# Performance work log

Measured on AMD Instinct MI355X. Metric: run time of the kernel, lower is better.

The kernel has to match this reference:

```python
import math
import jax, jax.numpy as jnp
import numpy as np

B, T, D = 4, 4096, 512


def setup_inputs() -> dict:
    key = jax.random.key(0)
    k1, _ = jax.random.split(key)
    x = jax.random.normal(k1, (B, T, D), dtype=jnp.float32)
    log_alpha = jnp.zeros((), dtype=jnp.float32)
    return {"x": x, "log_alpha": log_alpha}


def _gelu_tanh(x):
    c = math.sqrt(2.0 / math.pi)
    return 0.5 * x * (1.0 + jnp.tanh(c * (x + 0.044715 * x * x * x)))


def reference(x, log_alpha):
    Bx, Tx, Dx = x.shape
    alpha = jax.nn.softplus(log_alpha)
    # F.normalize(dim=-1): x / max(||x||, eps)
    norm = jnp.maximum(jnp.linalg.norm(x, axis=-1, keepdims=True), 1e-12)
    x_norm = x / norm
    sim = jnp.einsum("btd,bsd->bts", x_norm, x_norm)  # [B,T,T]
    # causal mask: triu incl. diagonal (col >= row) filled with -2.0
    row = jnp.arange(Tx)[:, None]
    col = jnp.arange(Tx)[None, :]
    mask = col >= row  # [T,T]
    sim = jnp.where(mask[None], jnp.float32(-2.0), sim)
    max_sim = jnp.max(sim, axis=-1)  # [B,T]
    max_sim = jnp.maximum(max_sim, -1.0)
    familiarity = (max_sim + 1.0) * 0.5
    novelty = 1.0 - familiarity
    gate = 1.0 + alpha * novelty[..., None]  # [B,T,1]
    return _gelu_tanh(x * gate)
```

## Files before the change

### kernel.cpp

```cpp
#include <hip/hip_runtime.h>
#include <hip/hip_bf16.h>
#include <math.h>

#define B_ 4
#define T_ 4096
#define D_ 512
#define BT 128
#define BK 32
#define STEPS (D_ / BK)
#define NT (T_ / BT)
#define NPAIR (NT * (NT + 1) / 2)


typedef short bf16x8 __attribute__((ext_vector_type(8)));
typedef float f32x4 __attribute__((ext_vector_type(4)));

__device__ __forceinline__ unsigned short f2bf(float f) {
    unsigned u = __float_as_uint(f);
    u += 0x7FFFu + ((u >> 16) & 1u);
    return (unsigned short)(u >> 16);
}
__device__ __forceinline__ unsigned f2ord(float f) {
    unsigned u = __float_as_uint(f);
    return (u & 0x80000000u) ? ~u : (u | 0x80000000u);
}
__device__ __forceinline__ float ord2f(unsigned u) {
    unsigned b = (u & 0x80000000u) ? (u ^ 0x80000000u) : ~u;
    return __uint_as_float(b);
}

__device__ __forceinline__ void async16(const unsigned short* g, unsigned short* l) {
    __builtin_amdgcn_global_load_lds(
        (const __attribute__((address_space(1))) unsigned int*)g,
        (__attribute__((address_space(3))) unsigned int*)l, 16, 0, 0);
}

__global__ __launch_bounds__(256) void k_norm(const float* __restrict__ x,
                                              unsigned short* __restrict__ xn,
                                              unsigned* __restrict__ maxsim) {
    int w = (blockIdx.x * 256 + threadIdx.x) >> 6;
    int lane = threadIdx.x & 63;
    const float4* xr = (const float4*)(x + (size_t)w * D_);
    float4 a = xr[lane];
    float4 b = xr[lane + 64];
    float ss = a.x * a.x + a.y * a.y + a.z * a.z + a.w * a.w +
               b.x * b.x + b.y * b.y + b.z * b.z + b.w * b.w;
#pragma unroll
    for (int off = 32; off > 0; off >>= 1) ss += __shfl_xor(ss, off);
    float inv = 1.0f / fmaxf(sqrtf(ss), 1e-12f);
    unsigned u0 = (unsigned)f2bf(a.x * inv) | ((unsigned)f2bf(a.y * inv) << 16);
    unsigned u1 = (unsigned)f2bf(a.z * inv) | ((unsigned)f2bf(a.w * inv) << 16);
    unsigned u2 = (unsigned)f2bf(b.x * inv) | ((unsigned)f2bf(b.y * inv) << 16);
    unsigned u3 = (unsigned)f2bf(b.z * inv) | ((unsigned)f2bf(b.w * inv) << 16);
    uint2* xo = (uint2*)(xn + (size_t)w * D_);
    xo[lane]      = make_uint2(u0, u1);
    xo[lane + 64] = make_uint2(u2, u3);
    if (lane == 0) maxsim[w] = f2ord(-2.0f);
}

__global__ __launch_bounds__(256) void k_maxsim(const unsigned short* __restrict__ xn,
                                                unsigned* __restrict__ maxsim) {
    __shared__ __align__(16) unsigned short Buf[3][8192];
    const int b = blockIdx.y;
    const int p = blockIdx.x;
    int ti = (int)((sqrtf(8.0f * (float)p + 1.0f) - 1.0f) * 0.5f);
    while ((ti + 1) * (ti + 2) / 2 <= p) ti++;
    while (ti * (ti + 1) / 2 > p) ti--;
    const int si = p - ti * (ti + 1) / 2;
    const int t0 = ti * BT, s0 = si * BT;

    const int tid = threadIdx.x;
    const int wave = tid >> 6, lane = tid & 63;
    const int wm = wave >> 1, wn = wave & 1;
    const int qa = lane >> 4, la = lane & 15;
    const int swz = (la >> 1) & 3;

    const unsigned short* Ab = xn + (size_t)(b * T_ + t0) * D_;
    const unsigned short* Bb = xn + (size_t)(b * T_ + s0) * D_;

    const int c0 = tid,        r0_ = c0 >> 2, g0 = (c0 & 3) ^ ((r0_ >> 1) & 3);
    const int c1 = 256 + tid,  r1_ = c1 >> 2, g1 = (c1 & 3) ^ ((r1_ >> 1) & 3);
    const unsigned short* gA0 = Ab + (size_t)r0_ * D_ + g0 * 8;
    const unsigned short* gA1 = Ab + (size_t)r1_ * D_ + g1 * 8;
    const unsigned short* gB0 = Bb + (size_t)r0_ * D_ + g0 * 8;
    const unsigned short* gB1 = Bb + (size_t)r1_ * D_ + g1 * 8;
    const int ldsb0 = (wave * 64) * 8;
    const int ldsb1 = (256 + wave * 64) * 8;

#define STAGE(step, st)                                            \
    do {                                                           \
        async16(gA0 + (step) * BK, &Buf[st][ldsb0]);               \
        async16(gB0 + (step) * BK, &Buf[st][4096 + ldsb0]);        \
        async16(gA1 + (step) * BK, &Buf[st][ldsb1]);               \
        async16(gB1 + (step) * BK, &Buf[st][4096 + ldsb1]);        \
    } while (0)

    f32x4 acc[4][4];
#pragma unroll
    for (int i = 0; i < 4; i++)
#pragma unroll
        for (int j = 0; j < 4; j++) acc[i][j] = (f32x4){0.f, 0.f, 0.f, 0.f};

    STAGE(0, 0);
    STAGE(1, 1);

#pragma unroll
    for (int k = 0; k < STEPS; ++k) {
        const int cur = k % 3;
        if (k == STEPS - 1) __builtin_amdgcn_s_waitcnt(0x0F70);
        else                __builtin_amdgcn_s_waitcnt(0x0F74);
        __builtin_amdgcn_s_barrier();
        __asm__ __volatile__("" ::: "memory");
        if (k + 2 < STEPS) STAGE(k + 2, (k + 2) % 3);

        const unsigned short* As = &Buf[cur][0];
        const unsigned short* Bs = &Buf[cur][4096];
        bf16x8 af[4], bfr[4];
#pragma unroll
        for (int i = 0; i < 4; i++)
            af[i] = *(const bf16x8*)&As[(wm * 64 + i * 16 + la) * BK + (qa ^ swz) * 8];
#pragma unroll
        for (int j = 0; j < 4; j++)
            bfr[j] = *(const bf16x8*)&Bs[(wn * 64 + j * 16 + la) * BK + (qa ^ swz) * 8];
#pragma unroll
        for (int i = 0; i < 4; i++)
#pragma unroll
            for (int j = 0; j < 4; j++)
                acc[i][j] = __builtin_amdgcn_mfma_f32_16x16x32_bf16(af[i], bfr[j], acc[i][j], 0, 0, 0);
    }
#undef STAGE

    const bool diag = (ti == si);
#pragma unroll
    for (int i = 0; i < 4; i++) {
#pragma unroll
        for (int r = 0; r < 4; r++) {
            int tl = wm * 64 + i * 16 + qa * 4 + r;
            float m = -2.0f;
#pragma unroll
            for (int j = 0; j < 4; j++) {
                int sl = wn * 64 + j * 16 + la;
                float v = acc[i][j][r];
                if (!diag || sl < tl) m = fmaxf(m, v);
            }
#pragma unroll
            for (int off = 1; off < 16; off <<= 1) m = fmaxf(m, __shfl_xor(m, off));
            if (la == 0) atomicMax(&maxsim[b * T_ + t0 + tl], f2ord(m));
        }
    }
}

__device__ __forceinline__ float gelu_tanh(float y) {
    float t = tanhf(0.7978845608028654f * (y + 0.044715f * y * y * y));
    return 0.5f * y * (1.0f + t);
}

__global__ __launch_bounds__(256) void k_gate(const float* __restrict__ x,
                                              const float* __restrict__ log_alpha,
                                              const unsigned* __restrict__ maxsim,
                                              float* __restrict__ out) {
    int idx = blockIdx.x * 256 + threadIdx.x;
    float la = log_alpha[0];
    float alpha = (la > 20.0f) ? la : log1pf(expf(la));
    int row = idx >> 7;
    float m = fmaxf(ord2f(maxsim[row]), -1.0f);
    float novelty = 1.0f - (m + 1.0f) * 0.5f;
    float gate = 1.0f + alpha * novelty;
    float4 v = ((const float4*)x)[idx];
    float4 o;
    o.x = gelu_tanh(v.x * gate);
    o.y = gelu_tanh(v.y * gate);
    o.z = gelu_tanh(v.z * gate);
    o.w = gelu_tanh(v.w * gate);
    ((float4*)out)[idx] = o;
}

extern "C" void kernel_launch(void* const* d_in, const int* in_sizes, int n_in,
                              void* d_out, int out_size, void* d_ws, size_t ws_size,
                              hipStream_t stream) {
    const float* x = (const float*)d_in[0];
    const float* log_alpha = (const float*)d_in[1];
    float* out = (float*)d_out;

    unsigned* maxsim = (unsigned*)d_ws;
    unsigned short* xn = (unsigned short*)((char*)d_ws + 65536);

    const int rows = B_ * T_;
    k_norm<<<rows / 4, 256, 0, stream>>>(x, xn, maxsim);

    dim3 g2(NPAIR, B_);
    k_maxsim<<<g2, 256, 0, stream>>>(xn, maxsim);

    k_gate<<<(B_ * T_ * D_ / 4) / 256, 256, 0, stream>>>(x, log_alpha, maxsim, out);
}
```

Before: 144.2 us.

## Quantize normalized rows to FP8 and use FP8 MFMA for similarity

```diff
diff --git a/kernel.cpp b/kernel.cpp
--- a/kernel.cpp
+++ b/kernel.cpp
@@ -6,20 +6,14 @@
 #define T_ 4096
 #define D_ 512
 #define BT 128
-#define BK 32
+#define BK 64
 #define STEPS (D_ / BK)
 #define NT (T_ / BT)
 #define NPAIR (NT * (NT + 1) / 2)
 
 
-typedef short bf16x8 __attribute__((ext_vector_type(8)));
 typedef float f32x4 __attribute__((ext_vector_type(4)));
 
-__device__ __forceinline__ unsigned short f2bf(float f) {
-    unsigned u = __float_as_uint(f);
-    u += 0x7FFFu + ((u >> 16) & 1u);
-    return (unsigned short)(u >> 16);
-}
 __device__ __forceinline__ unsigned f2ord(float f) {
     unsigned u = __float_as_uint(f);
     return (u & 0x80000000u) ? ~u : (u | 0x80000000u);
@@ -29,14 +23,14 @@
     return __uint_as_float(b);
 }
 
-__device__ __forceinline__ void async16(const unsigned short* g, unsigned short* l) {
+__device__ __forceinline__ void async16(const unsigned char* g, unsigned char* l) {
     __builtin_amdgcn_global_load_lds(
         (const __attribute__((address_space(1))) unsigned int*)g,
         (__attribute__((address_space(3))) unsigned int*)l, 16, 0, 0);
 }
 
 __global__ __launch_bounds__(256) void k_norm(const float* __restrict__ x,
-                                              unsigned short* __restrict__ xn,
+                                              unsigned char* __restrict__ xn,
                                               unsigned* __restrict__ maxsim) {
     int w = (blockIdx.x * 256 + threadIdx.x) >> 6;
     int lane = threadIdx.x & 63;
@@ -48,19 +42,19 @@
 #pragma unroll
     for (int off = 32; off > 0; off >>= 1) ss += __shfl_xor(ss, off);
     float inv = 1.0f / fmaxf(sqrtf(ss), 1e-12f);
-    unsigned u0 = (unsigned)f2bf(a.x * inv) | ((unsigned)f2bf(a.y * inv) << 16);
-    unsigned u1 = (unsigned)f2bf(a.z * inv) | ((unsigned)f2bf(a.w * inv) << 16);
-    unsigned u2 = (unsigned)f2bf(b.x * inv) | ((unsigned)f2bf(b.y * inv) << 16);
-    unsigned u3 = (unsigned)f2bf(b.z * inv) | ((unsigned)f2bf(b.w * inv) << 16);
-    uint2* xo = (uint2*)(xn + (size_t)w * D_);
-    xo[lane]      = make_uint2(u0, u1);
-    xo[lane + 64] = make_uint2(u2, u3);
+    int u0 = __builtin_amdgcn_cvt_pk_fp8_f32(a.x * inv, a.y * inv, 0, false);
+    u0 = __builtin_amdgcn_cvt_pk_fp8_f32(a.z * inv, a.w * inv, u0, true);
+    int u1 = __builtin_amdgcn_cvt_pk_fp8_f32(b.x * inv, b.y * inv, 0, false);
+    u1 = __builtin_amdgcn_cvt_pk_fp8_f32(b.z * inv, b.w * inv, u1, true);
+    unsigned* xo = (unsigned*)(xn + (size_t)w * D_);
+    xo[lane]      = (unsigned)u0;
+    xo[lane + 64] = (unsigned)u1;
     if (lane == 0) maxsim[w] = f2ord(-2.0f);
 }
 
-__global__ __launch_bounds__(256) void k_maxsim(const unsigned short* __restrict__ xn,
+__global__ __launch_bounds__(256) void k_maxsim(const unsigned char* __restrict__ xn,
                                                 unsigned* __restrict__ maxsim) {
-    __shared__ __align__(16) unsigned short Buf[3][8192];
+    __shared__ __align__(16) unsigned char Buf[3][16384];
     const int b = blockIdx.y;
     const int p = blockIdx.x;
     int ti = (int)((sqrtf(8.0f * (float)p + 1.0f) - 1.0f) * 0.5f);
@@ -75,24 +69,24 @@
     const int qa = lane >> 4, la = lane & 15;
     const int swz = (la >> 1) & 3;
 
-    const unsigned short* Ab = xn + (size_t)(b * T_ + t0) * D_;
-    const unsigned short* Bb = xn + (size_t)(b * T_ + s0) * D_;
+    const unsigned char* Ab = xn + (size_t)(b * T_ + t0) * D_;
+    const unsigned char* Bb = xn + (size_t)(b * T_ + s0) * D_;
 
-    const int c0 = tid,        r0_ = c0 >> 2, g0 = (c0 & 3) ^ ((r0_ >> 1) & 3);
-    const int c1 = 256 + tid,  r1_ = c1 >> 2, g1 = (c1 & 3) ^ ((r1_ >> 1) & 3);
-    const unsigned short* gA0 = Ab + (size_t)r0_ * D_ + g0 * 8;
-    const unsigned short* gA1 = Ab + (size_t)r1_ * D_ + g1 * 8;
-    const unsigned short* gB0 = Bb + (size_t)r0_ * D_ + g0 * 8;
-    const unsigned short* gB1 = Bb + (size_t)r1_ * D_ + g1 * 8;
-    const int ldsb0 = (wave * 64) * 8;
-    const int ldsb1 = (256 + wave * 64) * 8;
+    const int c0 = tid,       r0_ = c0 >> 2, g0 = (c0 & 3) ^ ((r0_ >> 1) & 3);
+    const int c1 = 256 + tid, r1_ = c1 >> 2, g1 = (c1 & 3) ^ ((r1_ >> 1) & 3);
+    const unsigned char* gA0 = Ab + (size_t)r0_ * D_ + g0 * 16;
+    const unsigned char* gA1 = Ab + (size_t)r1_ * D_ + g1 * 16;
+    const unsigned char* gB0 = Bb + (size_t)r0_ * D_ + g0 * 16;
+    const unsigned char* gB1 = Bb + (size_t)r1_ * D_ + g1 * 16;
+    const int ldsb0 = (wave * 64) * 16;
+    const int ldsb1 = (256 + wave * 64) * 16;
 
 #define STAGE(step, st)                                            \
     do {                                                           \
         async16(gA0 + (step) * BK, &Buf[st][ldsb0]);               \
-        async16(gB0 + (step) * BK, &Buf[st][4096 + ldsb0]);        \
+        async16(gB0 + (step) * BK, &Buf[st][8192 + ldsb0]);        \
         async16(gA1 + (step) * BK, &Buf[st][ldsb1]);               \
-        async16(gB1 + (step) * BK, &Buf[st][4096 + ldsb1]);        \
+        async16(gB1 + (step) * BK, &Buf[st][8192 + ldsb1]);        \
     } while (0)
 
     f32x4 acc[4][4];
@@ -100,6 +94,9 @@
     for (int i = 0; i < 4; i++)
 #pragma unroll
         for (int j = 0; j < 4; j++) acc[i][j] = (f32x4){0.f, 0.f, 0.f, 0.f};
+
+    const int poff0 = (((qa >> 1) ^ swz) * 16) + (qa & 1) * 8;
+    const int poff1 = ((((qa >> 1) + 2) ^ swz) * 16) + (qa & 1) * 8;
 
     STAGE(0, 0);
     STAGE(1, 1);
@@ -113,20 +110,25 @@
         __asm__ __volatile__("" ::: "memory");
         if (k + 2 < STEPS) STAGE(k + 2, (k + 2) % 3);
 
-        const unsigned short* As = &Buf[cur][0];
-        const unsigned short* Bs = &Buf[cur][4096];
-        bf16x8 af[4], bfr[4];
+        const unsigned char* As = &Buf[cur][0];
+        const unsigned char* Bs = &Buf[cur][8192];
 #pragma unroll
-        for (int i = 0; i < 4; i++)
-            af[i] = *(const bf16x8*)&As[(wm * 64 + i * 16 + la) * BK + (qa ^ swz) * 8];
+        for (int h = 0; h < 2; h++) {
+            const int poff = h ? poff1 : poff0;
+            long af[4], bfr[4];
 #pragma unroll
-        for (int j = 0; j < 4; j++)
-            bfr[j] = *(const bf16x8*)&Bs[(wn * 64 + j * 16 + la) * BK + (qa ^ swz) * 8];
-#pragma unroll
-        for (int i = 0; i < 4; i++)
+            for (int i = 0; i < 4; i++)
+                af[i] = *(const long*)&As[(wm * 64 + i * 16 + la) * 64 + poff];
 #pragma unroll
             for (int j = 0; j < 4; j++)
-                acc[i][j] = __builtin_amdgcn_mfma_f32_16x16x32_bf16(af[i], bfr[j], acc[i][j], 0, 0, 0);
+                bfr[j] = *(const long*)&Bs[(wn * 64 + j * 16 + la) * 64 + poff];
+#pragma unroll
+            for (int i = 0; i < 4; i++)
+#pragma unroll
+                for (int j = 0; j < 4; j++)
+                    acc[i][j] = __builtin_amdgcn_mfma_f32_16x16x32_fp8_fp8(
+                        af[i], bfr[j], acc[i][j], 0, 0, 0);
+        }
     }
 #undef STAGE
 
@@ -183,7 +185,7 @@
     float* out = (float*)d_out;
 
     unsigned* maxsim = (unsigned*)d_ws;
-    unsigned short* xn = (unsigned short*)((char*)d_ws + 65536);
+    unsigned char* xn = (unsigned char*)d_ws + 65536;
 
     const int rows = B_ * T_;
     k_norm<<<rows / 4, 256, 0, stream>>>(x, xn, maxsim);
```

After: 133.6 us. 7.3% less time.
